# Performance work log

Measured on AMD Instinct MI355X. Metric: run time of the kernel, lower is better.

Reference implementation:

```python
import jax, jax.numpy as jnp
import numpy as np

BS, S, H = 32, 2048, 1024

def setup_inputs() -> dict:
    key = jax.random.key(0)
    k1, k2, k3, k4 = jax.random.split(key, 4)
    hidden = jax.random.normal(k1, (BS, H), dtype=jnp.float32)
    encoder_outputs = jax.random.normal(k2, (BS, S, H), dtype=jnp.float32)
    # nn.Linear(H, H): weight [H, H], bias [H], kaiming-uniform-ish init
    bound = 1.0 / np.sqrt(H)
    W = jax.random.uniform(k3, (H, H), dtype=jnp.float32, minval=-bound, maxval=bound)
    b = jax.random.uniform(k4, (H,), dtype=jnp.float32, minval=-bound, maxval=bound)
    return {"hidden": hidden, "encoder_outputs": encoder_outputs, "W": W, "b": b}

def reference(hidden, encoder_outputs, W, b):
    # energy_i = Linear(enc_i); score_i = sum(hidden * energy_i); softmax over seq
    energy = jnp.einsum('bsh,kh->bsk', encoder_outputs, W) + b  # [BS, S, H]
    scores = jnp.einsum('bsh,bh->bs', energy, hidden)           # [BS, S]
    return jax.nn.softmax(scores, axis=-1)
```

## Files before the change

kernel.cpp:

```cpp
#include <hip/hip_runtime.h>
#include <math.h>

#define BS 32
#define S  2048
#define H  1024

__global__ __launch_bounds__(256) void compute_v(const float* __restrict__ hidden,
                                                 const float* __restrict__ W,
                                                 float* __restrict__ v) {
    __shared__ float hid[H];
    __shared__ float part[4][64];
    const int b    = blockIdx.y;
    const int tid  = threadIdx.x;
    const int wave = tid >> 6;
    const int lane = tid & 63;

    ((float4*)hid)[tid] = ((const float4*)(hidden + b * H))[tid];
    __syncthreads();

    const int h = blockIdx.x * 64 + lane;
    const float* Wp = W + (size_t)(wave * 256) * H + h;
    const float* hp = hid + wave * 256;
    float acc = 0.f;
#pragma unroll 8
    for (int k = 0; k < 256; ++k)
        acc = fmaf(Wp[(size_t)k * H], hp[k], acc);

    part[wave][lane] = acc;
    __syncthreads();
    if (wave == 0) {
        float r = (part[0][lane] + part[1][lane]) + (part[2][lane] + part[3][lane]);
        v[b * H + h] = r;
    }
}

__global__ __launch_bounds__(256) void compute_scores(const float* __restrict__ enc,
                                                      const float* __restrict__ v,
                                                      float* __restrict__ scores) {
    const int b    = blockIdx.y;
    const int tid  = threadIdx.x;
    const int wave = tid >> 6;
    const int lane = tid & 63;

    const float4* v4 = (const float4*)(v + b * H);
    float4 vr[4];
#pragma unroll
    for (int it = 0; it < 4; ++it) vr[it] = v4[it * 64 + lane];

    const int s0 = blockIdx.x * 64 + wave * 16;
    const float4* encb = (const float4*)enc + (size_t)b * S * (H / 4);

#pragma unroll
    for (int i = 0; i < 16; i += 8) {
        float acc[8] = {0.f, 0.f, 0.f, 0.f, 0.f, 0.f, 0.f, 0.f};
#pragma unroll
        for (int j = 0; j < 8; ++j) {
            const float4* e4 = encb + (size_t)(s0 + i + j) * (H / 4);
#pragma unroll
            for (int it = 0; it < 4; ++it) {
                float4 e = e4[it * 64 + lane];
                acc[j] = fmaf(e.x, vr[it].x, acc[j]);
                acc[j] = fmaf(e.y, vr[it].y, acc[j]);
                acc[j] = fmaf(e.z, vr[it].z, acc[j]);
                acc[j] = fmaf(e.w, vr[it].w, acc[j]);
            }
        }
#pragma unroll
        for (int off = 32; off > 0; off >>= 1) {
#pragma unroll
            for (int j = 0; j < 8; ++j)
                acc[j] += __shfl_xor(acc[j], off, 64);
        }
        if (lane < 8)
            scores[b * S + s0 + i + lane] = acc[lane];
    }
}

__global__ __launch_bounds__(256) void softmax_rows(float* __restrict__ scores) {
    const int b    = blockIdx.x;
    const int tid  = threadIdx.x;
    const int wave = tid >> 6;
    const int lane = tid & 63;
    __shared__ float red[4];

    float4* row4 = (float4*)(scores + b * S);
    float4 x[2];
    float m = -INFINITY;
#pragma unroll
    for (int i = 0; i < 2; ++i) {
        x[i] = row4[tid + i * 256];
        m = fmaxf(m, fmaxf(fmaxf(x[i].x, x[i].y), fmaxf(x[i].z, x[i].w)));
    }
#pragma unroll
    for (int off = 1; off < 64; off <<= 1)
        m = fmaxf(m, __shfl_xor(m, off, 64));
    if (lane == 0) red[wave] = m;
    __syncthreads();
    m = fmaxf(fmaxf(red[0], red[1]), fmaxf(red[2], red[3]));

    float sum = 0.f;
#pragma unroll
    for (int i = 0; i < 2; ++i) {
        x[i].x = __expf(x[i].x - m);
        x[i].y = __expf(x[i].y - m);
        x[i].z = __expf(x[i].z - m);
        x[i].w = __expf(x[i].w - m);
        sum += (x[i].x + x[i].y) + (x[i].z + x[i].w);
    }
#pragma unroll
    for (int off = 1; off < 64; off <<= 1)
        sum += __shfl_xor(sum, off, 64);
    __syncthreads();
    if (lane == 0) red[wave] = sum;
    __syncthreads();
    sum = (red[0] + red[1]) + (red[2] + red[3]);
    const float inv = 1.0f / sum;

#pragma unroll
    for (int i = 0; i < 2; ++i) {
        x[i].x *= inv; x[i].y *= inv; x[i].z *= inv; x[i].w *= inv;
        row4[tid + i * 256] = x[i];
    }
}

extern "C" void kernel_launch(void* const* d_in, const int* in_sizes, int n_in,
                              void* d_out, int out_size, void* d_ws, size_t ws_size,
                              hipStream_t stream) {
    const float* hidden = (const float*)d_in[0];
    const float* enc    = (const float*)d_in[1];
    const float* W      = (const float*)d_in[2];

    float* v    = (float*)d_ws;
    float* outp = (float*)d_out;

    dim3 g1(H / 64, BS);
    compute_v<<<g1, 256, 0, stream>>>(hidden, W, v);

    dim3 g2(S / 64, BS);
    compute_scores<<<g2, 256, 0, stream>>>(enc, v, outp);

    softmax_rows<<<BS, 256, 0, stream>>>(outp);
}
```

Baseline: 391.9 us.

## Fuse softmax into score kernel via last-block atomic counter, nontemporal loads

Removes the separate softmax launch: each score block bumps a per-batch atomic counter after a threadfence, and the last block to finish a row runs the softmax on it. The counters are zeroed inside compute_v. Encoder reads now use nontemporal loads, and the rows per inner batch drop from 8 to 4, which lowers register pressure. In exchange the softmax work runs serially in the tail blocks, and each block pays for a fence and an atomic.

```diff
diff --git a/kernel.cpp b/kernel.cpp
--- a/kernel.cpp
+++ b/kernel.cpp
@@ -5,15 +5,21 @@
 #define S  2048
 #define H  1024
 
+typedef float vfloat4 __attribute__((ext_vector_type(4)));
+
 __global__ __launch_bounds__(256) void compute_v(const float* __restrict__ hidden,
                                                  const float* __restrict__ W,
-                                                 float* __restrict__ v) {
+                                                 float* __restrict__ v,
+                                                 int* __restrict__ counters) {
     __shared__ float hid[H];
     __shared__ float part[4][64];
     const int b    = blockIdx.y;
     const int tid  = threadIdx.x;
     const int wave = tid >> 6;
     const int lane = tid & 63;
+
+    if (blockIdx.x == 0 && blockIdx.y == 0 && tid < BS)
+        counters[tid] = 0;
 
     ((float4*)hid)[tid] = ((const float4*)(hidden + b * H))[tid];
     __syncthreads();
@@ -34,9 +40,11 @@
     }
 }
 
-__global__ __launch_bounds__(256) void compute_scores(const float* __restrict__ enc,
-                                                      const float* __restrict__ v,
-                                                      float* __restrict__ scores) {
+__global__ __launch_bounds__(256) void compute_scores_softmax(
+        const float* __restrict__ enc,
+        const float* __restrict__ v,
+        float* __restrict__ scores,
+        int* __restrict__ counters) {
     const int b    = blockIdx.y;
     const int tid  = threadIdx.x;
     const int wave = tid >> 6;
@@ -48,17 +56,17 @@
     for (int it = 0; it < 4; ++it) vr[it] = v4[it * 64 + lane];
 
     const int s0 = blockIdx.x * 64 + wave * 16;
-    const float4* encb = (const float4*)enc + (size_t)b * S * (H / 4);
+    const vfloat4* encb = (const vfloat4*)enc + (size_t)b * S * (H / 4);
 
 #pragma unroll
-    for (int i = 0; i < 16; i += 8) {
-        float acc[8] = {0.f, 0.f, 0.f, 0.f, 0.f, 0.f, 0.f, 0.f};
+    for (int i = 0; i < 16; i += 4) {
+        float acc[4] = {0.f, 0.f, 0.f, 0.f};
 #pragma unroll
-        for (int j = 0; j < 8; ++j) {
-            const float4* e4 = encb + (size_t)(s0 + i + j) * (H / 4);
+        for (int j = 0; j < 4; ++j) {
+            const vfloat4* e4 = encb + (size_t)(s0 + i + j) * (H / 4);
 #pragma unroll
             for (int it = 0; it < 4; ++it) {
-                float4 e = e4[it * 64 + lane];
+                vfloat4 e = __builtin_nontemporal_load(&e4[it * 64 + lane]);
                 acc[j] = fmaf(e.x, vr[it].x, acc[j]);
                 acc[j] = fmaf(e.y, vr[it].y, acc[j]);
                 acc[j] = fmaf(e.z, vr[it].z, acc[j]);
@@ -68,21 +76,24 @@
 #pragma unroll
         for (int off = 32; off > 0; off >>= 1) {
 #pragma unroll
-            for (int j = 0; j < 8; ++j)
+            for (int j = 0; j < 4; ++j)
                 acc[j] += __shfl_xor(acc[j], off, 64);
         }
-        if (lane < 8)
+        if (lane < 4)
             scores[b * S + s0 + i + lane] = acc[lane];
     }
-}
 
-__global__ __launch_bounds__(256) void softmax_rows(float* __restrict__ scores) {
-    const int b    = blockIdx.x;
-    const int tid  = threadIdx.x;
-    const int wave = tid >> 6;
-    const int lane = tid & 63;
+    __threadfence();
+    __shared__ int is_last;
+    if (tid == 0) {
+        int old = atomicAdd(&counters[b], 1);
+        is_last = (old == (S / 64) - 1);
+    }
+    __syncthreads();
+    if (!is_last) return;
+    __threadfence();
+
     __shared__ float red[4];
-
     float4* row4 = (float4*)(scores + b * S);
     float4 x[2];
     float m = -INFINITY;
@@ -130,14 +141,13 @@
     const float* enc    = (const float*)d_in[1];
     const float* W      = (const float*)d_in[2];
 
-    float* v    = (float*)d_ws;
-    float* outp = (float*)d_out;
+    float* v        = (float*)d_ws;
+    int*   counters = (int*)((char*)d_ws + BS * H * sizeof(float));
+    float* outp     = (float*)d_out;
 
     dim3 g1(H / 64, BS);
-    compute_v<<<g1, 256, 0, stream>>>(hidden, W, v);
+    compute_v<<<g1, 256, 0, stream>>>(hidden, W, v, counters);
 
     dim3 g2(S / 64, BS);
-    compute_scores<<<g2, 256, 0, stream>>>(enc, v, outp);
-
-    softmax_rows<<<BS, 256, 0, stream>>>(outp);
+    compute_scores_softmax<<<g2, 256, 0, stream>>>(enc, v, outp, counters);
 }
```

Result: slower. 563.5 us (+43.8%).
